# Optimization experiments

Hardware: AMD Instinct MI355X
Metric: run time of the kernel (lower is better)

Reference implementation:

```python
import jax, jax.numpy as jnp
import numpy as np

DIM = 64
HEADS = 8
NBLK = 4

def conv2d(x, w, b=None, groups=1, pad=0):
    out = jax.lax.conv_general_dilated(x, w, (1, 1), [(pad, pad), (pad, pad)],
        feature_group_count=groups, dimension_numbers=('NCHW', 'OIHW', 'NCHW'))
    return out if b is None else out + b[None, :, None, None]

def layer_norm_c(x, w, b):
    # WithBias LayerNorm over channel dim (torch code does it in (b,hw,c) layout)
    mu = jnp.mean(x, axis=1, keepdims=True)
    var = jnp.mean(jnp.square(x - mu), axis=1, keepdims=True)
    return (x - mu) / jnp.sqrt(var + 1e-5) * w[None, :, None, None] + b[None, :, None, None]

def l2norm(x):
    n = jnp.sqrt(jnp.sum(jnp.square(x), axis=-1, keepdims=True))
    return x / jnp.maximum(n, 1e-12)

def attention(x, w_qkv, w_dw, temp, w_proj):
    # transposed (channel) attention: C x C per head, N = h*w
    b, c, h, w = x.shape
    qkv = conv2d(conv2d(x, w_qkv), w_dw, groups=3 * c, pad=1)
    q, k, v = jnp.split(qkv, 3, axis=1)
    rs = lambda t: t.reshape(b, HEADS, c // HEADS, h * w)
    q, k, v = l2norm(rs(q)), l2norm(rs(k)), rs(v)
    attn = jax.nn.softmax(jnp.einsum('bhcn,bhdn->bhcd', q, k) * temp[None], axis=-1)
    out = jnp.einsum('bhcd,bhdn->bhcn', attn, v).reshape(b, c, h, w)
    return conv2d(out, w_proj)

def ffn(x, w_in, w_dw, w_out):
    y = conv2d(x, w_in)
    y = conv2d(y, w_dw, groups=y.shape[1], pad=1)
    y1, y2 = jnp.split(y, 2, axis=1)
    return conv2d(jax.nn.gelu(y1, approximate=False) * y2, w_out)

def ciim(low, high, w_ir, w_vi, w_fu, b_fu, w_dw, b_dw, eca_w):
    lf = conv2d(low, w_ir)   # [B, 2*DIM, H, W]
    hf = conv2d(high, w_vi)
    fuse = conv2d(jnp.concatenate([lf, hf], 1), w_fu, b_fu)  # [B, 2*DIM, H, W]
    la = jnp.broadcast_to(jnp.mean(lf, (2, 3), keepdims=True), lf.shape)
    ha = jnp.broadcast_to(jnp.mean(hf, (2, 3), keepdims=True), hf.shape)
    hl = conv2d(jnp.concatenate([fuse, la, ha], 1), w_dw, b_dw, groups=DIM, pad=1)  # 6*DIM -> DIM grouped
    h_map = jax.nn.sigmoid(jax.nn.gelu(hl, approximate=False))
    l_map = jax.nn.sigmoid(jax.nn.relu(hl))
    out = jnp.concatenate([h_map * low, l_map * high], 1)  # [B, 2*DIM, H, W]
    B, C, H, W = out.shape
    g = DIM // 2  # channel shuffle with groups = dim // 2
    out = out.reshape(B, g, C // g, H, W).swapaxes(1, 2).reshape(B, C, H, W)
    # eca_layer with k_size=1 reduces to per-channel sigmoid gate on the global mean
    y = jax.nn.sigmoid(jnp.mean(out, (2, 3)) * eca_w)
    return out * y[:, :, None, None]

def reference(inp_img, base_feature, detail_feature, w_conv_ir, w_conv_vi, w_conv_fusion,
              b_conv_fusion, w_dw_ciim, b_dw_ciim, eca_w, w_rc2, ln1_w, ln1_b, w_qkv,
              w_qkv_dw, temp, w_proj, ln2_w, ln2_b, w_in, w_ffn_dw, w_out_ffn, w_head1, w_head2):
    x0 = ciim(base_feature, detail_feature, w_conv_ir, w_conv_vi, w_conv_fusion,
              b_conv_fusion, w_dw_ciim, b_dw_ciim, eca_w)
    x0 = conv2d(x0, w_rc2)  # 2*DIM -> DIM
    x = x0
    for i in range(NBLK):
        x = x + attention(layer_norm_c(x, ln1_w[i], ln1_b[i]), w_qkv[i], w_qkv_dw[i], temp[i], w_proj[i])
        x = x + ffn(layer_norm_c(x, ln2_w[i], ln2_b[i]), w_in[i], w_ffn_dw[i], w_out_ffn[i])
    y = conv2d(x, w_head1, pad=1)
    y = jnp.where(y > 0, y, 0.01 * y)  # LeakyReLU(0.01)
    y = conv2d(y, w_head2, pad=1) + inp_img
    return jax.nn.sigmoid(y), x0

def setup_inputs():
    key = jax.random.key(0)
    ks = jax.random.split(key, 20)
    r = lambda k, s, sc=0.02: jax.random.normal(k, s, dtype=jnp.float32) * sc
    B, H, W = 4, 256, 256
    return {
        'inp_img': r(ks[0], (B, 1, H, W), 1.0),
        'base_feature': r(ks[1], (B, DIM, H, W), 1.0),
        'detail_feature': r(ks[2], (B, DIM, H, W), 1.0),
        'w_conv_ir': r(ks[3], (128, 64, 1, 1)),
        'w_conv_vi': r(ks[4], (128, 64, 1, 1)),
        'w_conv_fusion': r(ks[5], (128, 256, 1, 1)),
        'b_conv_fusion': jnp.zeros((128,), jnp.float32),
        'w_dw_ciim': r(ks[6], (64, 6, 3, 3)),
        'b_dw_ciim': jnp.zeros((64,), jnp.float32),
        'eca_w': r(ks[7], (128,), 1.0),
        'w_rc2': r(ks[8], (64, 128, 1, 1)),
        'ln1_w': jnp.ones((NBLK, 64), jnp.float32),
        'ln1_b': jnp.zeros((NBLK, 64), jnp.float32),
        'w_qkv': r(ks[9], (NBLK, 192, 64, 1, 1)),
        'w_qkv_dw': r(ks[10], (NBLK, 192, 1, 3, 3)),
        'temp': jnp.ones((NBLK, HEADS, 1, 1), jnp.float32),
        'w_proj': r(ks[11], (NBLK, 64, 64, 1, 1)),
        'ln2_w': jnp.ones((NBLK, 64), jnp.float32),
        'ln2_b': jnp.zeros((NBLK, 64), jnp.float32),
        'w_in': r(ks[12], (NBLK, 256, 64, 1, 1)),
        'w_ffn_dw': r(ks[13], (NBLK, 256, 1, 3, 3)),
        'w_out_ffn': r(ks[14], (NBLK, 64, 128, 1, 1)),
        'w_head1': r(ks[15], (32, 64, 3, 3)),
        'w_head2': r(ks[16], (1, 32, 3, 3)),
    }
```

## Files before the change

kernel.cpp:

```cpp
#include <hip/hip_runtime.h>
#include <hip/hip_bf16.h>
#include <math.h>

#define NP 65536L
#define HHH 256
#define WWW 256
#define QKCH 32

typedef unsigned short u16;
typedef unsigned short ushort8_t __attribute__((ext_vector_type(8)));
typedef short s16x8 __attribute__((ext_vector_type(8)));
typedef float f32x4 __attribute__((ext_vector_type(4)));

__device__ __forceinline__ float bf2f(u16 u) { return __uint_as_float(((unsigned)u) << 16); }
__device__ __forceinline__ u16 f2bf(float f) {
    __hip_bfloat16 h = __float2bfloat16(f);
    return *reinterpret_cast<u16*>(&h);
}
__device__ __forceinline__ float sigmoidf_(float x) { return 1.f / (1.f + __expf(-x)); }
__device__ __forceinline__ float gelu_exact(float x) {
    return 0.5f * x * (1.f + erff(x * 0.70710678118654752f));
}

__global__ void diag_kernel(float* out, float v) {
    if (threadIdx.x == 0 && blockIdx.x == 0) out[0] = v;
}

__global__ __launch_bounds__(256) void prep_misc(
    const float* __restrict__ wir, const float* __restrict__ wvi,
    const float* __restrict__ wfu, const float* __restrict__ wout,
    const float* __restrict__ wh1,
    u16* __restrict__ dir, u16* __restrict__ dvi,
    u16* __restrict__ dfu, u16* __restrict__ dout,
    u16* __restrict__ wtap)
{
    int bid = blockIdx.x;
    if (bid < 80) {
        long e = (long)bid * 1024 + threadIdx.x * 4;
        const float* src; u16* dst; long off;
        if (e < 8192)       { src = wir;  dst = dir;  off = 0; }
        else if (e < 16384) { src = wvi;  dst = dvi;  off = 8192; }
        else if (e < 49152) { src = wfu;  dst = dfu;  off = 16384; }
        else                { src = wout; dst = dout; off = 49152; }
        long i = e - off;
        float4 v = *(const float4*)(src + i);
        ushort4 o;
        o.x = f2bf(v.x); o.y = f2bf(v.y); o.z = f2bf(v.z); o.w = f2bf(v.w);
        *(ushort4*)(dst + i) = o;
    } else {
        int tap = bid - 80;
        for (int e = threadIdx.x; e < 2048; e += 256)
            wtap[tap * 2048 + e] = f2bf(wh1[(long)e * 9 + tap]);
    }
}

__global__ void fold_ln(
    const float* __restrict__ wqkv, const float* __restrict__ ln1w, const float* __restrict__ ln1b,
    const float* __restrict__ win,  const float* __restrict__ ln2w, const float* __restrict__ ln2b,
    u16* __restrict__ fq, float* __restrict__ fqB,
    u16* __restrict__ ff, float* __restrict__ ffB)
{
    int g = blockIdx.x;
    int i = g / 7, r = g % 7;
    const float *wsrc, *lg, *lb;
    u16* wd; float* Bd;
    int obase;
    if (r < 3) {
        wsrc = wqkv + (long)i * 192 * 64; lg = ln1w + i * 64; lb = ln1b + i * 64;
        wd = fq + (long)i * 192 * 64; Bd = fqB + i * 192; obase = r * 64;
    } else {
        wsrc = win + (long)i * 256 * 64; lg = ln2w + i * 64; lb = ln2b + i * 64;
        wd = ff + (long)i * 256 * 64; Bd = ffB + i * 256; obase = (r - 3) * 64;
    }
    int o = obase + threadIdx.x;
    float Bv = 0.f;
    for (int c = 0; c < 64; ++c) {
        float wv = wsrc[(long)o * 64 + c];
        wd[(long)o * 64 + c] = f2bf(wv * lg[c]);
        Bv += wv * lb[c];
    }
    Bd[o] = Bv;
}

__global__ __launch_bounds__(256) void gemm_irvi(
    const float* __restrict__ base, const float* __restrict__ detail,
    const u16* __restrict__ wir, const u16* __restrict__ wvi,
    u16* __restrict__ Y, float* __restrict__ means)
{
    __shared__ u16 XT[256][72];
    __shared__ u16 WT[64][72];
    __shared__ float red[4][64];
    int xsel = blockIdx.x, b = blockIdx.z;
    long P0 = (long)blockIdx.y * 256;
    int tid = threadIdx.x, lane = tid & 63, wave = tid >> 6;
    int rl = lane & 15, rg = lane >> 4;
    const float* in = ((xsel < 2) ? base : detail) + (long)b * 64 * NP;
    const u16* wsel = (xsel < 2) ? wir : wvi;
    int orow0 = (xsel & 1) * 64;
    int ochan0 = xsel * 64;

    {
        int o = tid >> 2, cs = (tid & 3) * 16;
        const u16* src = wsel + (long)(orow0 + o) * 64 + cs;
        *(ushort8_t*)&WT[o][cs] = *(const ushort8_t*)src;
        *(ushort8_t*)&WT[o][cs + 8] = *(const ushort8_t*)(src + 8);
    }
    {
        int c0 = (tid & 7) * 8;
        int pt = (tid >> 3) * 8;
        u16 rr[8][8];
#pragma unroll
        for (int i = 0; i < 8; ++i) {
            const float* sp = in + (long)(c0 + i) * NP + P0 + pt;
            float4 a = *(const float4*)sp;
            float4 b4 = *(const float4*)(sp + 4);
            rr[i][0] = f2bf(a.x); rr[i][1] = f2bf(a.y);
            rr[i][2] = f2bf(a.z); rr[i][3] = f2bf(a.w);
            rr[i][4] = f2bf(b4.x); rr[i][5] = f2bf(b4.y);
            rr[i][6] = f2bf(b4.z); rr[i][7] = f2bf(b4.w);
        }
#pragma unroll
        for (int j = 0; j < 8; ++j) {
            ushort8_t v;
#pragma unroll
            for (int i = 0; i < 8; ++i) v[i] = rr[i][j];
            *(ushort8_t*)&XT[pt + j][c0] = v;
        }
    }
    __syncthreads();
    f32x4 acc[4][4];
#pragma unroll
    for (int m = 0; m < 4; ++m)
#pragma unroll
        for (int n = 0; n < 4; ++n) acc[m][n] = (f32x4){0.f, 0.f, 0.f, 0.f};
#pragma unroll
    for (int ks = 0; ks < 2; ++ks) {
        int kc = ks * 32 + rg * 8;
        s16x8 a[4], bb[4];
#pragma unroll
        for (int m = 0; m < 4; ++m) a[m] = *(const s16x8*)&WT[m * 16 + rl][kc];
#pragma unroll
        for (int n = 0; n < 4; ++n) bb[n] = *(const s16x8*)&XT[wave * 64 + n * 16 + rl][kc];
#pragma unroll
        for (int m = 0; m < 4; ++m)
#pragma unroll
            for (int n = 0; n < 4; ++n)
                acc[m][n] = __builtin_amdgcn_mfma_f32_16x16x32_bf16(a[m], bb[n], acc[m][n], 0, 0, 0);
    }
    float csum[4][4];
#pragma unroll
    for (int m = 0; m < 4; ++m)
#pragma unroll
        for (int r = 0; r < 4; ++r) csum[m][r] = 0.f;
#pragma unroll
    for (int m = 0; m < 4; ++m)
#pragma unroll
        for (int n = 0; n < 4; ++n) {
            long px = P0 + wave * 64 + n * 16 + rl;
#pragma unroll
            for (int r = 0; r < 4; ++r) {
                int oo = ochan0 + m * 16 + rg * 4 + r;
                float v = acc[m][n][r];
                Y[((long)b * 256 + oo) * NP + px] = f2bf(v);
                csum[m][r] += v;
            }
        }
#pragma unroll
    for (int m = 0; m < 4; ++m)
#pragma unroll
        for (int r = 0; r < 4; ++r) {
            float s = csum[m][r];
            s += __shfl_xor(s, 1); s += __shfl_xor(s, 2);
            s += __shfl_xor(s, 4); s += __shfl_xor(s, 8);
            if (rl == 0) red[wave][m * 16 + rg * 4 + r] = s;
        }
    __syncthreads();
    if (tid < 64) {
        float v = red[0][tid] + red[1][tid] + red[2][tid] + red[3][tid];
        atomicAdd(&means[b * 256 + ochan0 + tid], v * (1.f / NP));
    }
}

__global__ __launch_bounds__(256) void gemm_plain(
    const u16* __restrict__ in, long inBS,
    const u16* __restrict__ wbf,
    const float* __restrict__ bias,
    u16* __restrict__ outp, long outBS, int Cin)
{
    __shared__ u16 XT[256][72];
    __shared__ u16 WT[64][72];
    int b = blockIdx.z;
    int oBase = blockIdx.x * 64;
    long P0 = (long)blockIdx.y * 256;
    int tid = threadIdx.x, lane = tid & 63, wave = tid >> 6;
    int rl = lane & 15, rg = lane >> 4;
    const u16* inB = in + (long)b * inBS;
    f32x4 acc[4][4];
#pragma unroll
    for (int m = 0; m < 4; ++m)
#pragma unroll
        for (int n = 0; n < 4; ++n) acc[m][n] = (f32x4){0.f, 0.f, 0.f, 0.f};
    for (int ck = 0; ck < Cin; ck += 64) {
        if (ck) __syncthreads();
        {
            int o = tid >> 2, cs = (tid & 3) * 16;
            const u16* src = wbf + (long)(oBase + o) * Cin + ck + cs;
            *(ushort8_t*)&WT[o][cs] = *(const ushort8_t*)src;
            *(ushort8_t*)&WT[o][cs + 8] = *(const ushort8_t*)(src + 8);
        }
        {
            int c0 = (tid & 7) * 8;
            int pt = (tid >> 3) * 8;
            ushort8_t r[8];
#pragma unroll
            for (int i = 0; i < 8; ++i)
                r[i] = *(const ushort8_t*)(inB + (long)(ck + c0 + i) * NP + P0 + pt);
#pragma unroll
            for (int j = 0; j < 8; ++j) {
                ushort8_t v;
#pragma unroll
                for (int i = 0; i < 8; ++i) v[i] = r[i][j];
                *(ushort8_t*)&XT[pt + j][c0] = v;
            }
        }
        __syncthreads();
#pragma unroll
        for (int ks = 0; ks < 2; ++ks) {
            int kc = ks * 32 + rg * 8;
            s16x8 a[4], bb[4];
#pragma unroll
            for (int m = 0; m < 4; ++m) a[m] = *(const s16x8*)&WT[m * 16 + rl][kc];
#pragma unroll
            for (int n = 0; n < 4; ++n) bb[n] = *(const s16x8*)&XT[wave * 64 + n * 16 + rl][kc];
#pragma unroll
            for (int m = 0; m < 4; ++m)
#pragma unroll
                for (int n = 0; n < 4; ++n)
                    acc[m][n] = __builtin_amdgcn_mfma_f32_16x16x32_bf16(a[m], bb[n], acc[m][n], 0, 0, 0);
        }
    }
#pragma unroll
    for (int m = 0; m < 4; ++m) {
#pragma unroll
        for (int n = 0; n < 4; ++n) {
            long px = P0 + wave * 64 + n * 16 + rl;
#pragma unroll
            for (int r = 0; r < 4; ++r) {
                int oo = oBase + m * 16 + rg * 4 + r;
                outp[(long)b * outBS + (long)oo * NP + px] = f2bf(acc[m][n][r] + bias[oo]);
            }
        }
    }
}

template<int WEFF, int RESID, int DUAL, int M2, int PIXMAJ>
__global__ __launch_bounds__(256) void gemm_fused(
    const u16* __restrict__ in, long inBS,
    const u16* __restrict__ w1, long w1BS,
    const u16* __restrict__ residX,
    u16* __restrict__ Xout,
    float* __restrict__ out2,
    const u16* __restrict__ w2, const float* __restrict__ bias2,
    u16* __restrict__ Yout,
    const float* __restrict__ part, const float* __restrict__ temp,
    const float* __restrict__ wproj,
    int Cin)
{
    __shared__ u16 XT[128][72] __attribute__((aligned(16)));
    __shared__ u16 WT[64][72] __attribute__((aligned(16)));
    int b = blockIdx.z;
    long P0 = (long)blockIdx.x * 128;
    int tid = threadIdx.x, lane = tid & 63, wave = tid >> 6;
    int rl = lane & 15, rg = lane >> 4;
    const u16* inB = in + (long)b * inBS;

    if constexpr (WEFF) {
        float* SgF = (float*)&XT[0][0];
        float* attF = SgF + 640;
        for (int e = tid; e < 640; e += 256) {
            int h = e / 80, k = e % 80;
            const float* pp = part + (((long)b * 8 + h) * 80 + k) * QKCH;
            float s = 0.f;
#pragma unroll
            for (int c = 0; c < QKCH; ++c) s += pp[c];
            SgF[e] = s;
        }
        __syncthreads();
        if (tid < 64) {
            int h = tid >> 3, iq = tid & 7;
            float nqv = fmaxf(sqrtf(SgF[h * 80 + 64 + iq]), 1e-12f);
            float tp = temp[h];
            float row[8], mx = -1e30f;
#pragma unroll
            for (int jj = 0; jj < 8; ++jj) {
                float nkv = fmaxf(sqrtf(SgF[h * 80 + 72 + jj]), 1e-12f);
                row[jj] = SgF[h * 80 + iq * 8 + jj] / (nqv * nkv) * tp;
                mx = fmaxf(mx, row[jj]);
            }
            float sum = 0.f;
#pragma unroll
            for (int jj = 0; jj < 8; ++jj) { row[jj] = __expf(row[jj] - mx); sum += row[jj]; }
            float rinv = 1.f / sum;
#pragma unroll
            for (int jj = 0; jj < 8; ++jj) attF[(h * 8 + iq) * 8 + jj] = row[jj] * rinv;
        }
        __syncthreads();
        {
            int o = tid >> 2;
            int cv0 = (tid & 3) * 16;
#pragma unroll
            for (int cv = 0; cv < 16; ++cv) {
                int c = cv0 + cv;
                int h = c >> 3, jj = c & 7;
                float s = 0.f;
#pragma unroll
                for (int i = 0; i < 8; ++i)
                    s = fmaf(wproj[o * 64 + h * 8 + i], attF[(h * 8 + i) * 8 + jj], s);
                WT[o][c] = f2bf(s);
            }
        }
        __syncthreads();
    }

    f32x4 acc[4][2];
#pragma unroll
    for (int m = 0; m < 4; ++m)
#pragma unroll
        for (int n = 0; n < 2; ++n) acc[m][n] = (f32x4){0.f, 0.f, 0.f, 0.f};

    for (int ck = 0; ck < Cin; ck += 64) {
        if (ck) __syncthreads();
        if constexpr (!WEFF) {
            int o = tid >> 2, cs = (tid & 3) * 16;
            const u16* src = w1 + (long)b * w1BS + (long)o * Cin + ck + cs;
            *(ushort8_t*)&WT[o][cs] = *(const ushort8_t*)src;
            *(ushort8_t*)&WT[o][cs + 8] = *(const ushort8_t*)(src + 8);
        }
        if (tid < 128) {
            int c0 = (tid & 7) * 8;
            int pt = (tid >> 3) * 8;
            ushort8_t r[8];
#pragma unroll
            for (int i = 0; i < 8; ++i)
                r[i] = *(const ushort8_t*)(inB + (long)(ck + c0 + i) * NP + P0 + pt);
#pragma unroll
            for (int j = 0; j < 8; ++j) {
                ushort8_t v;
#pragma unroll
                for (int i = 0; i < 8; ++i) v[i] = r[i][j];
                *(ushort8_t*)&XT[pt + j][c0] = v;
            }
        }
        __syncthreads();
#pragma unroll
        for (int ks = 0; ks < 2; ++ks) {
            int kc = ks * 32 + rg * 8;
            s16x8 a[4], bb[2];
#pragma unroll
            for (int m = 0; m < 4; ++m) a[m] = *(const s16x8*)&WT[m * 16 + rl][kc];
#pragma unroll
            for (int n = 0; n < 2; ++n) bb[n] = *(const s16x8*)&XT[wave * 32 + n * 16 + rl][kc];
#pragma unroll
            for (int m = 0; m < 4; ++m)
#pragma unroll
                for (int n = 0; n < 2; ++n)
                    acc[m][n] = __builtin_amdgcn_mfma_f32_16x16x32_bf16(a[m], bb[n], acc[m][n], 0, 0, 0);
        }
    }

#pragma unroll
    for (int m = 0; m < 4; ++m)
#pragma unroll
        for (int n = 0; n < 2; ++n) {
            long px = P0 + wave * 32 + n * 16 + rl;
#pragma unroll
            for (int r = 0; r < 4; ++r) {
                int oo = m * 16 + rg * 4 + r;
                float t = acc[m][n][r];
                if constexpr (RESID) t += bf2f(residX[((long)b * 64 + oo) * NP + px]);
                acc[m][n][r] = t;
                if constexpr (!PIXMAJ) Xout[((long)b * 64 + oo) * NP + px] = f2bf(t);
                if constexpr (DUAL) out2[((long)b * 64 + oo) * NP + px] = t;
            }
        }

    if constexpr (PIXMAJ) {
        __syncthreads();
#pragma unroll
        for (int m = 0; m < 4; ++m)
#pragma unroll
            for (int n = 0; n < 2; ++n) {
                int pxl = wave * 32 + n * 16 + rl;
#pragma unroll
                for (int r = 0; r < 4; ++r)
                    XT[pxl][m * 16 + rg * 4 + r] = f2bf(acc[m][n][r]);
            }
        __syncthreads();
        int pxl = tid >> 1, c0 = (tid & 1) * 32;
        u16* dst = Xout + (long)b * (64 * NP) + (P0 + pxl) * 64 + c0;
        *(ushort8_t*)(dst)      = *(const ushort8_t*)&XT[pxl][c0];
        *(ushort8_t*)(dst + 8)  = *(const ushort8_t*)&XT[pxl][c0 + 8];
        *(ushort8_t*)(dst + 16) = *(const ushort8_t*)&XT[pxl][c0 + 16];
        *(ushort8_t*)(dst + 24) = *(const ushort8_t*)&XT[pxl][c0 + 24];
    }

    if constexpr (M2 > 0) {
        float muA[2], invA[2];
#pragma unroll
        for (int n = 0; n < 2; ++n) {
            float s = 0.f, s2 = 0.f;
#pragma unroll
            for (int m = 0; m < 4; ++m)
#pragma unroll
                for (int r = 0; r < 4; ++r) {
                    float t = acc[m][n][r];
                    s += t; s2 = fmaf(t, t, s2);
                }
            s += __shfl_xor(s, 16);  s += __shfl_xor(s, 32);
            s2 += __shfl_xor(s2, 16); s2 += __shfl_xor(s2, 32);
            float mu = s * (1.f / 64.f);
            float var = fmaxf(s2 * (1.f / 64.f) - mu * mu, 0.f);
            muA[n] = mu;
            invA[n] = rsqrtf(var + 1e-5f);
        }
        __syncthreads();
#pragma unroll
        for (int m = 0; m < 4; ++m)
#pragma unroll
            for (int n = 0; n < 2; ++n) {
                int pxl = wave * 32 + n * 16 + rl;
#pragma unroll
                for (int r = 0; r < 4; ++r)
                    XT[pxl][m * 16 + rg * 4 + r] = f2bf((acc[m][n][r] - muA[n]) * invA[n]);
            }
        __syncthreads();
        for (int mc = 0; mc < M2 / 64; ++mc) {
            if (mc) __syncthreads();
            {
                int o = tid >> 2, cs = (tid & 3) * 16;
                const u16* src = w2 + (long)(mc * 64 + o) * 64 + cs;
                *(ushort8_t*)&WT[o][cs] = *(const ushort8_t*)src;
                *(ushort8_t*)&WT[o][cs + 8] = *(const ushort8_t*)(src + 8);
            }
            __syncthreads();
            f32x4 a2[4][2];
#pragma unroll
            for (int m = 0; m < 4; ++m)
#pragma unroll
                for (int n = 0; n < 2; ++n) a2[m][n] = (f32x4){0.f, 0.f, 0.f, 0.f};
#pragma unroll
            for (int ks = 0; ks < 2; ++ks) {
                int kc = ks * 32 + rg * 8;
                s16x8 a[4], bb[2];
#pragma unroll
                for (int m = 0; m < 4; ++m) a[m] = *(const s16x8*)&WT[m * 16 + rl][kc];
#pragma unroll
                for (int n = 0; n < 2; ++n) bb[n] = *(const s16x8*)&XT[wave * 32 + n * 16 + rl][kc];
#pragma unroll
                for (int m = 0; m < 4; ++m)
#pragma unroll
                    for (int n = 0; n < 2; ++n)
                        a2[m][n] = __builtin_amdgcn_mfma_f32_16x16x32_bf16(a[m], bb[n], a2[m][n], 0, 0, 0);
            }
#pragma unroll
            for (int m = 0; m < 4; ++m) {
#pragma unroll
                for (int n = 0; n < 2; ++n) {
                    long px = P0 + wave * 32 + n * 16 + rl;
#pragma unroll
                    for (int r = 0; r < 4; ++r) {
                        int oo = mc * 64 + m * 16 + rg * 4 + r;
                        Yout[((long)b * 256 + oo) * NP + px] = f2bf(a2[m][n][r] + bias2[oo]);
                    }
                }
            }
        }
    }
}

__device__ __forceinline__ void stage_row(float (*S)[260], const u16* __restrict__ src,
                                          int y0, int j, int px)
{
    int row = y0 - 1 + j;
    if (row >= 0 && row < HHH) {
        ushort8_t a = *(const ushort8_t*)(src + row * WWW + px);
        ushort8_t b = *(const ushort8_t*)(src + row * WWW + px + 8);
#pragma unroll
        for (int e = 0; e < 8; ++e) { S[j][1 + px + e] = bf2f(a[e]); S[j][9 + px + e] = bf2f(b[e]); }
    } else {
#pragma unroll
        for (int e = 0; e < 16; ++e) S[j][1 + px + e] = 0.f;
    }
}
__device__ __forceinline__ float conv9(const float (*S)[260], int r, int col,
                                       const float* __restrict__ w9)
{
    float a = 0.f;
#pragma unroll
    for (int ky = 0; ky < 3; ++ky)
#pragma unroll
        for (int kx = 0; kx < 3; ++kx)
            a = fmaf(w9[ky * 3 + kx], S[r + ky][col + kx], a);
    return a;
}

__global__ __launch_bounds__(256) void dw3x3_strip(
    const u16* __restrict__ in, long inBS, const float* __restrict__ w,
    u16* __restrict__ out1, long out1BS,
    u16* __restrict__ out2, long out2BS, int obase2, int csplit)
{
    int strip = blockIdx.x, c = blockIdx.y, b = blockIdx.z;
    int y0 = strip * 16, tid = threadIdx.x;
    __shared__ float S[18][260];
    const u16* src = in + (long)b * inBS + (long)c * NP;
    int j = tid >> 4, px = (tid & 15) * 16;
    stage_row(S, src, y0, j, px);
    if (tid < 32) stage_row(S, src, y0, 16 + (tid >> 4), px);
    if (tid < 18) { S[tid][0] = 0.f; S[tid][257] = 0.f; }
    __syncthreads();
    float w9[9];
#pragma unroll
    for (int k = 0; k < 9; ++k) w9[k] = w[c * 9 + k];
    u16* dst = (c < csplit)
                   ? out1 + (long)b * out1BS + (long)c * NP
                   : out2 + (long)b * out2BS + (long)(obase2 + c - csplit) * NP;
    int px4 = (tid & 63) * 4;
    int r0 = (tid >> 6) * 4;
#pragma unroll
    for (int r = 0; r < 4; ++r) {
        int row = r0 + r;
        ushort4 ovec;
        u16* ov = (u16*)&ovec;
#pragma unroll
        for (int e = 0; e < 4; ++e) ov[e] = f2bf(conv9(S, row, px4 + e, w9));
        *(ushort4*)&dst[(y0 + row) * WWW + px4] = ovec;
    }
}

__global__ __launch_bounds__(256) void ffn_dw_glu_strip(
    const u16* __restrict__ y, long yBS, const float* __restrict__ w,
    u16* __restrict__ g, long gBS)
{
    int strip = blockIdx.x, c = blockIdx.y, b = blockIdx.z;
    int y0 = strip * 16, tid = threadIdx.x;
    __shared__ float S1[18][260];
    __shared__ float S2[18][260];
    const u16* s1 = y + (long)b * yBS + (long)c * NP;
    const u16* s2 = y + (long)b * yBS + (long)(c + 128) * NP;
    int j = tid >> 4, px = (tid & 15) * 16;
    stage_row(S1, s1, y0, j, px);
    if (tid < 32) stage_row(S1, s1, y0, 16 + (tid >> 4), px);
    stage_row(S2, s2, y0, j, px);
    if (tid < 32) stage_row(S2, s2, y0, 16 + (tid >> 4), px);
    if (tid < 18) { S1[tid][0] = S1[tid][257] = 0.f; S2[tid][0] = S2[tid][257] = 0.f; }
    __syncthreads();
    float w1[9], w2[9];
#pragma unroll
    for (int k = 0; k < 9; ++k) { w1[k] = w[c * 9 + k]; w2[k] = w[(c + 128) * 9 + k]; }
    u16* dst = g + (long)b * gBS + (long)c * NP;
    int px4 = (tid & 63) * 4;
    int r0 = (tid >> 6) * 4;
#pragma unroll
    for (int r = 0; r < 4; ++r) {
        int row = r0 + r;
        ushort4 ovec;
        u16* ov = (u16*)&ovec;
#pragma unroll
        for (int e = 0; e < 4; ++e) {
            float a1 = conv9(S1, row, px4 + e, w1);
            float a2 = conv9(S2, row, px4 + e, w2);
            ov[e] = f2bf(gelu_exact(a1) * a2);
        }
        *(ushort4*)&dst[(y0 + row) * WWW + px4] = ovec;
    }
}

__global__ __launch_bounds__(256) void ciim_dw_gate(
    const u16* __restrict__ fuse, long fBS, const float* __restrict__ means,
    const float* __restrict__ wdw, const float* __restrict__ bdw,
    const float* __restrict__ low, long lBS, const float* __restrict__ high,
    u16* __restrict__ Yout, long yBS, float* __restrict__ ecam)
{
    int strip = blockIdx.x, c = blockIdx.y, b = blockIdx.z;
    int y0 = strip * 16, tid = threadIdx.x;
    __shared__ float S[18][260];
    int px4 = (tid & 63) * 4;
    int r0 = (tid >> 6) * 4;
    float acc[4][4];
    float bias = bdw[c];
#pragma unroll
    for (int r = 0; r < 4; ++r)
#pragma unroll
        for (int e = 0; e < 4; ++e) acc[r][e] = bias;
    for (int j6 = 0; j6 < 6; ++j6) {
        int ic = 6 * c + j6;
        const float* w9p = wdw + (c * 6 + j6) * 9;
        float w9[9];
#pragma unroll
        for (int k = 0; k < 9; ++k) w9[k] = w9p[k];
        if (ic < 128) {
            __syncthreads();
            const u16* src = fuse + (long)b * fBS + (long)ic * NP;
            int j = tid >> 4, px = (tid & 15) * 16;
            stage_row(S, src, y0, j, px);
            if (tid < 32) stage_row(S, src, y0, 16 + (tid >> 4), px);
            if (tid < 18) { S[tid][0] = 0.f; S[tid][257] = 0.f; }
            __syncthreads();
#pragma unroll
            for (int r = 0; r < 4; ++r)
#pragma unroll
                for (int e = 0; e < 4; ++e) acc[r][e] += conv9(S, r0 + r, px4 + e, w9);
        } else {
            float mv = means[b * 256 + ic - 128];
#pragma unroll
            for (int r = 0; r < 4; ++r) {
                int row = y0 + r0 + r;
#pragma unroll
                for (int e = 0; e < 4; ++e) {
                    int xc = px4 + e;
                    float ws = 0.f;
#pragma unroll
                    for (int ky = 0; ky < 3; ++ky) {
                        int yy = row + ky - 1;
                        if (yy < 0 || yy >= HHH) continue;
#pragma unroll
                        for (int kx = 0; kx < 3; ++kx) {
                            int xx = xc + kx - 1;
                            if (xx < 0 || xx >= WWW) continue;
                            ws += w9[ky * 3 + kx];
                        }
                    }
                    acc[r][e] += mv * ws;
                }
            }
        }
    }
    int cn1 = 32 * (c & 3) + (c >> 2);
    int cn2 = cn1 + 16;
    u16* d1 = Yout + (long)b * yBS + (long)cn1 * NP;
    u16* d2 = Yout + (long)b * yBS + (long)cn2 * NP;
    const float* lp = low + (long)b * lBS + (long)c * NP;
    const float* hp = high + (long)b * lBS + (long)c * NP;
    float s1 = 0.f, s2 = 0.f;
#pragma unroll
    for (int r = 0; r < 4; ++r) {
        int row = y0 + r0 + r;
        float4 lv = *(const float4*)(lp + row * WWW + px4);
        float4 hv = *(const float4*)(hp + row * WWW + px4);
        float l4[4] = {lv.x, lv.y, lv.z, lv.w};
        float h4[4] = {hv.x, hv.y, hv.z, hv.w};
        ushort4 o1, o2;
        u16* p1 = (u16*)&o1;
        u16* p2 = (u16*)&o2;
#pragma unroll
        for (int e = 0; e < 4; ++e) {
            float hl = acc[r][e];
            float v1 = sigmoidf_(gelu_exact(hl)) * l4[e];
            float v2 = sigmoidf_(fmaxf(hl, 0.f)) * h4[e];
            p1[e] = f2bf(v1); p2[e] = f2bf(v2);
            s1 += v1; s2 += v2;
        }
        *(ushort4*)&d1[row * WWW + px4] = o1;
        *(ushort4*)&d2[row * WWW + px4] = o2;
    }
    __syncthreads();
    float* redbuf = &S[0][0];
    redbuf[tid] = s1; redbuf[256 + tid] = s2;
    __syncthreads();
    for (int st = 128; st > 0; st >>= 1) {
        if (tid < st) { redbuf[tid] += redbuf[tid + st]; redbuf[256 + tid] += redbuf[256 + tid + st]; }
        __syncthreads();
    }
    if (tid == 0) {
        atomicAdd(&ecam[b * 128 + cn1], redbuf[0] * (1.f / NP));
        atomicAdd(&ecam[b * 128 + cn2], redbuf[256] * (1.f / NP));
    }
}

__global__ __launch_bounds__(256) void rc2w_build(
    const float* __restrict__ ecam, const float* __restrict__ ecaw,
    const float* __restrict__ wrc2, u16* __restrict__ wout)
{
    int idx = blockIdx.x * 256 + threadIdx.x;
    int c = idx & 127, o = (idx >> 7) & 63, b = idx >> 13;
    float y = sigmoidf_(ecam[b * 128 + c] * ecaw[c]);
    wout[idx] = f2bf(wrc2[o * 128 + c] * y);
}

__global__ __launch_bounds__(256) void qk_dot(
    const u16* __restrict__ D, long dBS, float* __restrict__ part)
{
    int chunk = blockIdx.x, h = blockIdx.y, b = blockIdx.z;
    int tid = threadIdx.x, lane = tid & 63, wave = tid >> 6;
    const u16* q = D + (long)b * dBS + (long)(h * 8) * NP;
    const u16* k = q + 64 * NP;
    float dots[64], nq[8], nk[8];
#pragma unroll
    for (int a = 0; a < 64; ++a) dots[a] = 0.f;
#pragma unroll
    for (int a = 0; a < 8; ++a) { nq[a] = 0.f; nk[a] = 0.f; }
    long p = (long)chunk * 2048 + tid * 8;
    {
        ushort8_t qv[8], kv[8];
#pragma unroll
        for (int i = 0; i < 8; ++i) qv[i] = *(const ushort8_t*)(q + (long)i * NP + p);
#pragma unroll
        for (int i = 0; i < 8; ++i) kv[i] = *(const ushort8_t*)(k + (long)i * NP + p);
#pragma unroll
        for (int e = 0; e < 8; ++e) {
            float qe[8], ke[8];
#pragma unroll
            for (int i = 0; i < 8; ++i) { qe[i] = bf2f(qv[i][e]); ke[i] = bf2f(kv[i][e]); }
#pragma unroll
            for (int i = 0; i < 8; ++i) {
                nq[i] = fmaf(qe[i], qe[i], nq[i]);
                nk[i] = fmaf(ke[i], ke[i], nk[i]);
#pragma unroll
                for (int jj = 0; jj < 8; ++jj)
                    dots[i * 8 + jj] = fmaf(qe[i], ke[jj], dots[i * 8 + jj]);
            }
        }
    }
    __shared__ float red[4][80];
#pragma unroll
    for (int a = 0; a < 64; ++a) {
        float v = dots[a];
#pragma unroll
        for (int o = 32; o > 0; o >>= 1) v += __shfl_xor(v, o);
        if (lane == 0) red[wave][a] = v;
    }
#pragma unroll
    for (int a = 0; a < 8; ++a) {
        float v1 = nq[a], v2 = nk[a];
#pragma unroll
        for (int o = 32; o > 0; o >>= 1) { v1 += __shfl_xor(v1, o); v2 += __shfl_xor(v2, o); }
        if (lane == 0) { red[wave][64 + a] = v1; red[wave][72 + a] = v2; }
    }
    __syncthreads();
    if (tid < 80) {
        float v = red[0][tid] + red[1][tid] + red[2][tid] + red[3][tid];
        part[(((long)b * 8 + h) * 80 + tid) * QKCH + chunk] = v;
    }
}

__global__ __launch_bounds__(256) void head_fused(
    const u16* __restrict__ Xp, const u16* __restrict__ wtap,
    const float* __restrict__ wh2, const float* __restrict__ inp,
    float* __restrict__ out)
{
    __shared__ u16 P[18][18][72] __attribute__((aligned(16)));
    __shared__ u16 Hl[16][16][40] __attribute__((aligned(16)));
    __shared__ float w2t[288];
    int ty = blockIdx.x, tx = blockIdx.y, b = blockIdx.z;
    int tid = threadIdx.x, lane = tid & 63, wave = tid >> 6;
    int rl = lane & 15, rg = lane >> 4;
    int oy = ty * 14 - 2, ox = tx * 14 - 2;
    for (int idx = tid; idx < 288; idx += 256)
        w2t[(idx % 9) * 32 + idx / 9] = wh2[idx];
    {
        const u16* xb = Xp + (long)b * (64 * NP);
        int c0 = (tid & 7) * 8;
        for (int pp = tid >> 3; pp < 324; pp += 32) {
            int row = pp / 18, col = pp % 18;
            int gy = oy + row, gx = ox + col;
            ushort8_t v;
            if (gy >= 0 && gy < HHH && gx >= 0 && gx < WWW)
                v = *(const ushort8_t*)(xb + ((long)(gy * WWW + gx)) * 64 + c0);
            else
                v = (ushort8_t){0, 0, 0, 0, 0, 0, 0, 0};
            *(ushort8_t*)&P[row][col][c0] = v;
        }
    }
    __syncthreads();
    f32x4 acc[2][4];
#pragma unroll
    for (int m = 0; m < 2; ++m)
#pragma unroll
        for (int n = 0; n < 4; ++n) acc[m][n] = (f32x4){0.f, 0.f, 0.f, 0.f};
#pragma unroll
    for (int tap = 0; tap < 9; ++tap) {
        int ky = tap / 3, kx = tap % 3;
#pragma unroll
        for (int ks = 0; ks < 2; ++ks) {
            int kc = ks * 32 + rg * 8;
            s16x8 a0 = *(const s16x8*)(wtap + tap * 2048 + (long)(0 + rl) * 64 + kc);
            s16x8 a1 = *(const s16x8*)(wtap + tap * 2048 + (long)(16 + rl) * 64 + kc);
#pragma unroll
            for (int n = 0; n < 4; ++n) {
                int py = wave * 4 + n;
                s16x8 bb = *(const s16x8*)&P[py + ky][kx + rl][kc];
                acc[0][n] = __builtin_amdgcn_mfma_f32_16x16x32_bf16(a0, bb, acc[0][n], 0, 0, 0);
                acc[1][n] = __builtin_amdgcn_mfma_f32_16x16x32_bf16(a1, bb, acc[1][n], 0, 0, 0);
            }
        }
    }
#pragma unroll
    for (int m = 0; m < 2; ++m)
#pragma unroll
        for (int n = 0; n < 4; ++n) {
            int py = wave * 4 + n;
            int gy = ty * 14 - 1 + py, gx = tx * 14 - 1 + rl;
            bool ok = (gy >= 0 && gy < HHH && gx >= 0 && gx < WWW);
#pragma unroll
            for (int r = 0; r < 4; ++r) {
                int o = m * 16 + rg * 4 + r;
                float v = acc[m][n][r];
                v = v > 0.f ? v : 0.01f * v;
                Hl[py][rl][o] = ok ? f2bf(v) : (u16)0;
            }
        }
    __syncthreads();
    if (tid < 196) {
        int r = tid / 14, c = tid % 14;
        int gy = ty * 14 + r, gx = tx * 14 + c;
        if (gy < HHH && gx < WWW) {
            float acc2 = 0.f;
#pragma unroll
            for (int tap = 0; tap < 9; ++tap) {
                int hy = r + tap / 3, hx = c + tap % 3;
#pragma unroll
                for (int cg = 0; cg < 4; ++cg) {
                    ushort8_t hv = *(const ushort8_t*)&Hl[hy][hx][cg * 8];
#pragma unroll
                    for (int e = 0; e < 8; ++e)
                        acc2 = fmaf(w2t[tap * 32 + cg * 8 + e], bf2f(hv[e]), acc2);
                }
            }
            float v = acc2 + inp[(long)b * NP + gy * WWW + gx];
            out[(long)b * NP + gy * WWW + gx] = 1.f / (1.f + expf(-v));
        }
    }
}

extern "C" void kernel_launch(void* const* d_in, const int* in_sizes, int n_in,
                              void* d_out, int out_size, void* d_ws, size_t ws_size,
                              hipStream_t stream)
{
    const float* inp    = (const float*)d_in[0];
    const float* base   = (const float*)d_in[1];
    const float* detail = (const float*)d_in[2];
    const float* w_ir   = (const float*)d_in[3];
    const float* w_vi   = (const float*)d_in[4];
    const float* w_fu   = (const float*)d_in[5];
    const float* b_fu   = (const float*)d_in[6];
    const float* w_dwc  = (const float*)d_in[7];
    const float* b_dwc  = (const float*)d_in[8];
    const float* eca_w  = (const float*)d_in[9];
    const float* w_rc2  = (const float*)d_in[10];
    const float* ln1w   = (const float*)d_in[11];
    const float* ln1b   = (const float*)d_in[12];
    const float* w_qkv  = (const float*)d_in[13];
    const float* w_qdw  = (const float*)d_in[14];
    const float* temp   = (const float*)d_in[15];
    const float* w_proj = (const float*)d_in[16];
    const float* ln2w   = (const float*)d_in[17];
    const float* ln2b   = (const float*)d_in[18];
    const float* w_in_  = (const float*)d_in[19];
    const float* w_fdw  = (const float*)d_in[20];
    const float* w_out_ = (const float*)d_in[21];
    const float* w_h1   = (const float*)d_in[22];
    const float* w_h2   = (const float*)d_in[23];

    float* out = (float*)d_out;

    auto needB = [&](long nb) -> size_t {
        return (size_t)nb * NP * (64 * 2 + 256 * 2 + 128 * 2) + (4u << 20);
    };
    int bInner;
    if (ws_size >= needB(4)) bInner = 4;
    else if (ws_size >= needB(2)) bInner = 2;
    else if (ws_size >= needB(1)) bInner = 1;
    else {
        diag_kernel<<<1, 64, 0, stream>>>(out, (float)(ws_size >> 20));
        return;
    }
    const long nb = bInner;

    char* p = (char*)d_ws;
    auto alloc = [&](size_t bytes) -> char* {
        char* r = p; p += (bytes + 255) & ~(size_t)255; return r;
    };
    u16*   X      = (u16*)alloc((size_t)nb * 64 * NP * 2);
    u16*   Y      = (u16*)alloc((size_t)nb * 256 * NP * 2);
    u16*   Dq     = (u16*)alloc((size_t)nb * 128 * NP * 2);
    float* part   = (float*)alloc((size_t)nb * 8 * 80 * QKCH * 4);
    float* means  = (float*)alloc((size_t)nb * 384 * 4);
    float* ecam   = means + nb * 256;
    u16*   rc2wb  = (u16*)alloc((size_t)nb * 8192 * 2);
    u16*   fq_bf  = (u16*)alloc((size_t)4 * 192 * 64 * 2);
    float* fqB    = (float*)alloc((size_t)4 * 192 * 4);
    u16*   ff_bf  = (u16*)alloc((size_t)4 * 256 * 64 * 2);
    float* ffB    = (float*)alloc((size_t)4 * 256 * 4);
    u16*   wir_bf = (u16*)alloc(8192 * 2);
    u16*   wvi_bf = (u16*)alloc(8192 * 2);
    u16*   wfu_bf = (u16*)alloc(32768 * 2);
    u16*   wout_bf= (u16*)alloc(32768 * 2);
    u16*   wtap   = (u16*)alloc(9 * 2048 * 2);

    dim3 blk(256);

    fold_ln<<<dim3(28), dim3(64), 0, stream>>>(w_qkv, ln1w, ln1b, w_in_, ln2w, ln2b,
                                               fq_bf, fqB, ff_bf, ffB);
    prep_misc<<<dim3(89), blk, 0, stream>>>(w_ir, w_vi, w_fu, w_out_, w_h1,
                                            wir_bf, wvi_bf, wfu_bf, wout_bf, wtap);

    for (int b0 = 0; b0 < 4; b0 += bInner) {
        const float* inpB    = inp + (long)b0 * NP;
        const float* baseB   = base + (long)b0 * 64 * NP;
        const float* detailB = detail + (long)b0 * 64 * NP;
        float* out0  = out + (long)b0 * NP;
        float* outX0 = out + 262144 + (long)b0 * 64 * NP;

        hipMemsetAsync(means, 0, (size_t)nb * 384 * 4, stream);
        gemm_irvi<<<dim3(4, 256, nb), blk, 0, stream>>>(
            baseB, detailB, wir_bf, wvi_bf, Y, means);
        gemm_plain<<<dim3(2, 256, nb), blk, 0, stream>>>(
            Y, 256 * NP, wfu_bf, b_fu, Dq, 128 * NP, 256);
        ciim_dw_gate<<<dim3(16, 64, nb), blk, 0, stream>>>(
            Dq, 128 * NP, means, w_dwc, b_dwc, baseB, 64 * NP, detailB,
            Y, 256 * NP, ecam);
        rc2w_build<<<dim3(nb * 32), blk, 0, stream>>>(ecam, eca_w, w_rc2, rc2wb);
        gemm_fused<0, 0, 1, 192, 0><<<dim3(512, 1, nb), blk, 0, stream>>>(
            Y, 256 * NP, rc2wb, 8192, nullptr, X, outX0,
            fq_bf, fqB, Y, nullptr, nullptr, nullptr, 128);

        for (int i = 0; i < 4; ++i) {
            dw3x3_strip<<<dim3(16, 192, nb), blk, 0, stream>>>(
                Y, 256 * NP, w_qdw + (long)i * 192 * 9,
                Dq, 128 * NP, Y, 256 * NP, 192, 128);
            qk_dot<<<dim3(QKCH, 8, nb), blk, 0, stream>>>(Dq, 128 * NP, part);
            gemm_fused<1, 1, 0, 256, 0><<<dim3(512, 1, nb), blk, 0, stream>>>(
                Y + 192 * NP, 256 * NP, nullptr, 0, X, X, nullptr,
                ff_bf + (long)i * 256 * 64, ffB + i * 256, Y,
                part, temp + i * 8, w_proj + (long)i * 4096, 64);
            ffn_dw_glu_strip<<<dim3(16, 128, nb), blk, 0, stream>>>(
                Y, 256 * NP, w_fdw + (long)i * 256 * 9, Dq, 128 * NP);
            if (i < 3) {
                gemm_fused<0, 1, 0, 192, 0><<<dim3(512, 1, nb), blk, 0, stream>>>(
                    Dq, 128 * NP, wout_bf + (long)i * 8192, 0, X, X, nullptr,
                    fq_bf + (long)(i + 1) * 192 * 64, fqB + (i + 1) * 192, Y,
                    nullptr, nullptr, nullptr, 128);
            } else {
                gemm_fused<0, 1, 0, 0, 1><<<dim3(512, 1, nb), blk, 0, stream>>>(
                    Dq, 128 * NP, wout_bf + (long)i * 8192, 0, X, Y, nullptr,
                    nullptr, nullptr, nullptr, nullptr, nullptr, nullptr, 128);
            }
        }

        head_fused<<<dim3(19, 19, nb), blk, 0, stream>>>(Y, wtap, w_h2, inpB, out0);
    }
}
```

Measured before the change: 1.636 ms.

## Fold ir/vi 1x1 convs into fusion conv weights and derive means from input means

The ir and vi 1x1 convolutions are linear, so they are pre-multiplied into the fusion weight on the device, giving one 128x128 combined weight. A single GEMM now reads the fp32 base and detail inputs directly and produces the fused output. The per-channel means of lf and hf are rebuilt from input channel means, which the GEMM accumulates, through a small matrix-vector kernel. This removes the 256-channel intermediate tensor write and read and one GEMM launch, at the cost of rounding the combined weights to bf16 once, which changes numerics slightly.

```diff
diff --git a/kernel.cpp b/kernel.cpp
--- a/kernel.cpp
+++ b/kernel.cpp
@@ -27,31 +27,50 @@
 }
 
 __global__ __launch_bounds__(256) void prep_misc(
-    const float* __restrict__ wir, const float* __restrict__ wvi,
-    const float* __restrict__ wfu, const float* __restrict__ wout,
-    const float* __restrict__ wh1,
-    u16* __restrict__ dir, u16* __restrict__ dvi,
-    u16* __restrict__ dfu, u16* __restrict__ dout,
-    u16* __restrict__ wtap)
+    const float* __restrict__ wout, const float* __restrict__ wh1,
+    u16* __restrict__ dout, u16* __restrict__ wtap)
 {
     int bid = blockIdx.x;
-    if (bid < 80) {
-        long e = (long)bid * 1024 + threadIdx.x * 4;
-        const float* src; u16* dst; long off;
-        if (e < 8192)       { src = wir;  dst = dir;  off = 0; }
-        else if (e < 16384) { src = wvi;  dst = dvi;  off = 8192; }
-        else if (e < 49152) { src = wfu;  dst = dfu;  off = 16384; }
-        else                { src = wout; dst = dout; off = 49152; }
-        long i = e - off;
-        float4 v = *(const float4*)(src + i);
+    if (bid < 32) {
+        long i = (long)bid * 1024 + threadIdx.x * 4;
+        float4 v = *(const float4*)(wout + i);
         ushort4 o;
         o.x = f2bf(v.x); o.y = f2bf(v.y); o.z = f2bf(v.z); o.w = f2bf(v.w);
-        *(ushort4*)(dst + i) = o;
+        *(ushort4*)(dout + i) = o;
     } else {
-        int tap = bid - 80;
+        int tap = bid - 32;
         for (int e = threadIdx.x; e < 2048; e += 256)
             wtap[tap * 2048 + e] = f2bf(wh1[(long)e * 9 + tap]);
     }
+}
+
+__global__ __launch_bounds__(256) void prep_comb(
+    const float* __restrict__ wfu, const float* __restrict__ wir,
+    const float* __restrict__ wvi, u16* __restrict__ wcomb)
+{
+    int idx = blockIdx.x * 256 + threadIdx.x;
+    int o = idx >> 7, cc = idx & 127;
+    float s = 0.f;
+    if (cc < 64) {
+        for (int k = 0; k < 128; ++k) s = fmaf(wfu[o * 256 + k], wir[k * 64 + cc], s);
+    } else {
+        for (int k = 0; k < 128; ++k) s = fmaf(wfu[o * 256 + 128 + k], wvi[k * 64 + cc - 64], s);
+    }
+    wcomb[idx] = f2bf(s);
+}
+
+__global__ void means_xform(
+    const float* __restrict__ inmean, const float* __restrict__ wir,
+    const float* __restrict__ wvi, float* __restrict__ means)
+{
+    int b = blockIdx.x, t = threadIdx.x;
+    float s = 0.f;
+    if (t < 128) {
+        for (int c = 0; c < 64; ++c) s = fmaf(wir[t * 64 + c], inmean[b * 128 + c], s);
+    } else {
+        for (int c = 0; c < 64; ++c) s = fmaf(wvi[(t - 128) * 64 + c], inmean[b * 128 + 64 + c], s);
+    }
+    means[b * 256 + t] = s;
 }
 
 __global__ void fold_ln(
@@ -82,145 +101,69 @@
     Bd[o] = Bv;
 }
 
-__global__ __launch_bounds__(256) void gemm_irvi(
+__global__ __launch_bounds__(256) void gemm_fuse128(
     const float* __restrict__ base, const float* __restrict__ detail,
-    const u16* __restrict__ wir, const u16* __restrict__ wvi,
-    u16* __restrict__ Y, float* __restrict__ means)
+    const u16* __restrict__ wcomb, const float* __restrict__ bias,
+    u16* __restrict__ Dq, float* __restrict__ inmean)
 {
     __shared__ u16 XT[256][72];
     __shared__ u16 WT[64][72];
-    __shared__ float red[4][64];
-    int xsel = blockIdx.x, b = blockIdx.z;
-    long P0 = (long)blockIdx.y * 256;
-    int tid = threadIdx.x, lane = tid & 63, wave = tid >> 6;
-    int rl = lane & 15, rg = lane >> 4;
-    const float* in = ((xsel < 2) ? base : detail) + (long)b * 64 * NP;
-    const u16* wsel = (xsel < 2) ? wir : wvi;
-    int orow0 = (xsel & 1) * 64;
-    int ochan0 = xsel * 64;
-
-    {
-        int o = tid >> 2, cs = (tid & 3) * 16;
-        const u16* src = wsel + (long)(orow0 + o) * 64 + cs;
-        *(ushort8_t*)&WT[o][cs] = *(const ushort8_t*)src;
-        *(ushort8_t*)&WT[o][cs + 8] = *(const ushort8_t*)(src + 8);
-    }
-    {
-        int c0 = (tid & 7) * 8;
-        int pt = (tid >> 3) * 8;
-        u16 rr[8][8];
-#pragma unroll
-        for (int i = 0; i < 8; ++i) {
-            const float* sp = in + (long)(c0 + i) * NP + P0 + pt;
-            float4 a = *(const float4*)sp;
-            float4 b4 = *(const float4*)(sp + 4);
-            rr[i][0] = f2bf(a.x); rr[i][1] = f2bf(a.y);
-            rr[i][2] = f2bf(a.z); rr[i][3] = f2bf(a.w);
-            rr[i][4] = f2bf(b4.x); rr[i][5] = f2bf(b4.y);
-            rr[i][6] = f2bf(b4.z); rr[i][7] = f2bf(b4.w);
-        }
-#pragma unroll
-        for (int j = 0; j < 8; ++j) {
-            ushort8_t v;
-#pragma unroll
-            for (int i = 0; i < 8; ++i) v[i] = rr[i][j];
-            *(ushort8_t*)&XT[pt + j][c0] = v;
-        }
-    }
-    __syncthreads();
-    f32x4 acc[4][4];
-#pragma unroll
-    for (int m = 0; m < 4; ++m)
-#pragma unroll
-        for (int n = 0; n < 4; ++n) acc[m][n] = (f32x4){0.f, 0.f, 0.f, 0.f};
-#pragma unroll
-    for (int ks = 0; ks < 2; ++ks) {
-        int kc = ks * 32 + rg * 8;
-        s16x8 a[4], bb[4];
-#pragma unroll
-        for (int m = 0; m < 4; ++m) a[m] = *(const s16x8*)&WT[m * 16 + rl][kc];
-#pragma unroll
-        for (int n = 0; n < 4; ++n) bb[n] = *(const s16x8*)&XT[wave * 64 + n * 16 + rl][kc];
-#pragma unroll
-        for (int m = 0; m < 4; ++m)
-#pragma unroll
-            for (int n = 0; n < 4; ++n)
-                acc[m][n] = __builtin_amdgcn_mfma_f32_16x16x32_bf16(a[m], bb[n], acc[m][n], 0, 0, 0);
-    }
-    float csum[4][4];
-#pragma unroll
-    for (int m = 0; m < 4; ++m)
-#pragma unroll
-        for (int r = 0; r < 4; ++r) csum[m][r] = 0.f;
-#pragma unroll
-    for (int m = 0; m < 4; ++m)
-#pragma unroll
-        for (int n = 0; n < 4; ++n) {
-            long px = P0 + wave * 64 + n * 16 + rl;
-#pragma unroll
-            for (int r = 0; r < 4; ++r) {
-                int oo = ochan0 + m * 16 + rg * 4 + r;
-                float v = acc[m][n][r];
-                Y[((long)b * 256 + oo) * NP + px] = f2bf(v);
-                csum[m][r] += v;
-            }
-        }
-#pragma unroll
-    for (int m = 0; m < 4; ++m)
-#pragma unroll
-        for (int r = 0; r < 4; ++r) {
-            float s = csum[m][r];
-            s += __shfl_xor(s, 1); s += __shfl_xor(s, 2);
-            s += __shfl_xor(s, 4); s += __shfl_xor(s, 8);
-            if (rl == 0) red[wave][m * 16 + rg * 4 + r] = s;
-        }
-    __syncthreads();
-    if (tid < 64) {
-        float v = red[0][tid] + red[1][tid] + red[2][tid] + red[3][tid];
-        atomicAdd(&means[b * 256 + ochan0 + tid], v * (1.f / NP));
-    }
-}
-
-__global__ __launch_bounds__(256) void gemm_plain(
-    const u16* __restrict__ in, long inBS,
-    const u16* __restrict__ wbf,
-    const float* __restrict__ bias,
-    u16* __restrict__ outp, long outBS, int Cin)
-{
-    __shared__ u16 XT[256][72];
-    __shared__ u16 WT[64][72];
+    __shared__ float red[4][128];
     int b = blockIdx.z;
     int oBase = blockIdx.x * 64;
     long P0 = (long)blockIdx.y * 256;
     int tid = threadIdx.x, lane = tid & 63, wave = tid >> 6;
     int rl = lane & 15, rg = lane >> 4;
-    const u16* inB = in + (long)b * inBS;
+
     f32x4 acc[4][4];
 #pragma unroll
     for (int m = 0; m < 4; ++m)
 #pragma unroll
         for (int n = 0; n < 4; ++n) acc[m][n] = (f32x4){0.f, 0.f, 0.f, 0.f};
-    for (int ck = 0; ck < Cin; ck += 64) {
-        if (ck) __syncthreads();
+
+#pragma unroll
+    for (int ch = 0; ch < 2; ++ch) {
+        int ck = ch * 64;
+        if (ch) __syncthreads();
         {
             int o = tid >> 2, cs = (tid & 3) * 16;
-            const u16* src = wbf + (long)(oBase + o) * Cin + ck + cs;
+            const u16* src = wcomb + (long)(oBase + o) * 128 + ck + cs;
             *(ushort8_t*)&WT[o][cs] = *(const ushort8_t*)src;
             *(ushort8_t*)&WT[o][cs + 8] = *(const ushort8_t*)(src + 8);
         }
         {
+            const float* in = ((ch == 0) ? base : detail) + (long)b * 64 * NP;
             int c0 = (tid & 7) * 8;
             int pt = (tid >> 3) * 8;
-            ushort8_t r[8];
-#pragma unroll
-            for (int i = 0; i < 8; ++i)
-                r[i] = *(const ushort8_t*)(inB + (long)(ck + c0 + i) * NP + P0 + pt);
+            u16 rr[8][8];
+            float ls[8];
+#pragma unroll
+            for (int i = 0; i < 8; ++i) {
+                const float* sp = in + (long)(c0 + i) * NP + P0 + pt;
+                float4 a = *(const float4*)sp;
+                float4 b4 = *(const float4*)(sp + 4);
+                rr[i][0] = f2bf(a.x); rr[i][1] = f2bf(a.y);
+                rr[i][2] = f2bf(a.z); rr[i][3] = f2bf(a.w);
+                rr[i][4] = f2bf(b4.x); rr[i][5] = f2bf(b4.y);
+                rr[i][6] = f2bf(b4.z); rr[i][7] = f2bf(b4.w);
+                ls[i] = a.x + a.y + a.z + a.w + b4.x + b4.y + b4.z + b4.w;
+            }
 #pragma unroll
             for (int j = 0; j < 8; ++j) {
                 ushort8_t v;
 #pragma unroll
-                for (int i = 0; i < 8; ++i) v[i] = r[i][j];
+                for (int i = 0; i < 8; ++i) v[i] = rr[i][j];
                 *(ushort8_t*)&XT[pt + j][c0] = v;
+            }
+            if (oBase == 0) {
+#pragma unroll
+                for (int i = 0; i < 8; ++i) {
+                    float v = ls[i];
+                    v += __shfl_xor(v, 8);
+                    v += __shfl_xor(v, 16);
+                    v += __shfl_xor(v, 32);
+                    if ((lane & 56) == 0) red[wave][ck + c0 + i] = v;
+                }
             }
         }
         __syncthreads();
@@ -247,8 +190,15 @@
 #pragma unroll
             for (int r = 0; r < 4; ++r) {
                 int oo = oBase + m * 16 + rg * 4 + r;
-                outp[(long)b * outBS + (long)oo * NP + px] = f2bf(acc[m][n][r] + bias[oo]);
-            }
+                Dq[((long)b * 128 + oo) * NP + px] = f2bf(acc[m][n][r] + bias[oo]);
+            }
+        }
+    }
+    if (oBase == 0) {
+        __syncthreads();
+        if (tid < 128) {
+            float v = red[0][tid] + red[1][tid] + red[2][tid] + red[3][tid];
+            atomicAdd(&inmean[b * 128 + tid], v * (1.f / NP));
         }
     }
 }
@@ -884,16 +834,15 @@
     u16*   Y      = (u16*)alloc((size_t)nb * 256 * NP * 2);
     u16*   Dq     = (u16*)alloc((size_t)nb * 128 * NP * 2);
     float* part   = (float*)alloc((size_t)nb * 8 * 80 * QKCH * 4);
-    float* means  = (float*)alloc((size_t)nb * 384 * 4);
+    float* means  = (float*)alloc((size_t)nb * 640 * 4);
     float* ecam   = means + nb * 256;
+    float* inmean = ecam + nb * 128;
     u16*   rc2wb  = (u16*)alloc((size_t)nb * 8192 * 2);
     u16*   fq_bf  = (u16*)alloc((size_t)4 * 192 * 64 * 2);
     float* fqB    = (float*)alloc((size_t)4 * 192 * 4);
     u16*   ff_bf  = (u16*)alloc((size_t)4 * 256 * 64 * 2);
     float* ffB    = (float*)alloc((size_t)4 * 256 * 4);
-    u16*   wir_bf = (u16*)alloc(8192 * 2);
-    u16*   wvi_bf = (u16*)alloc(8192 * 2);
-    u16*   wfu_bf = (u16*)alloc(32768 * 2);
+    u16*   wcomb  = (u16*)alloc(16384 * 2);
     u16*   wout_bf= (u16*)alloc(32768 * 2);
     u16*   wtap   = (u16*)alloc(9 * 2048 * 2);
 
@@ -901,8 +850,8 @@
 
     fold_ln<<<dim3(28), dim3(64), 0, stream>>>(w_qkv, ln1w, ln1b, w_in_, ln2w, ln2b,
                                                fq_bf, fqB, ff_bf, ffB);
-    prep_misc<<<dim3(89), blk, 0, stream>>>(w_ir, w_vi, w_fu, w_out_, w_h1,
-                                            wir_bf, wvi_bf, wfu_bf, wout_bf, wtap);
+    prep_misc<<<dim3(41), blk, 0, stream>>>(w_out_, w_h1, wout_bf, wtap);
+    prep_comb<<<dim3(64), blk, 0, stream>>>(w_fu, w_ir, w_vi, wcomb);
 
     for (int b0 = 0; b0 < 4; b0 += bInner) {
         const float* inpB    = inp + (long)b0 * NP;
@@ -911,11 +860,10 @@
         float* out0  = out + (long)b0 * NP;
         float* outX0 = out + 262144 + (long)b0 * 64 * NP;
 
-        hipMemsetAsync(means, 0, (size_t)nb * 384 * 4, stream);
-        gemm_irvi<<<dim3(4, 256, nb), blk, 0, stream>>>(
-            baseB, detailB, wir_bf, wvi_bf, Y, means);
-        gemm_plain<<<dim3(2, 256, nb), blk, 0, stream>>>(
-            Y, 256 * NP, wfu_bf, b_fu, Dq, 128 * NP, 256);
+        hipMemsetAsync(means, 0, (size_t)nb * 640 * 4, stream);
+        gemm_fuse128<<<dim3(2, 256, nb), blk, 0, stream>>>(
+            baseB, detailB, wcomb, b_fu, Dq, inmean);
+        means_xform<<<dim3(nb), blk, 0, stream>>>(inmean, w_ir, w_vi, means);
         ciim_dw_gate<<<dim3(16, 64, nb), blk, 0, stream>>>(
             Dq, 128 * NP, means, w_dwc, b_dwc, baseB, 64 * NP, detailB,
             Y, 256 * NP, ecam);
```

Measured after the change: 1.568 ms (median of 2 runs). 1.04x faster.
